# Optimization experiments

Measured on AMD Instinct MI355X. Metric: run time of the kernel, lower is better.

Reference implementation:

```python
import jax, jax.numpy as jnp
import numpy as np

NUM_HEADS = 16
EPS = 1e-6


def _phi(x):
    # Positive feature map: ELU + 1
    return jax.nn.elu(x) + 1.0


def setup_inputs() -> dict:
    key = jax.random.key(0)
    ks = jax.random.split(key, 5)
    B, L, D = 4, 8192, 1024
    scale = 0.02
    return {
        "x": jax.random.normal(ks[0], (B, L, D), dtype=jnp.float32),
        "Wq": jax.random.normal(ks[1], (D, D), dtype=jnp.float32) * scale,
        "Wk": jax.random.normal(ks[2], (D, D), dtype=jnp.float32) * scale,
        "Wv": jax.random.normal(ks[3], (D, D), dtype=jnp.float32) * scale,
        "Wo": jax.random.normal(ks[4], (D, D), dtype=jnp.float32) * scale,
    }


def reference(x, Wq, Wk, Wv, Wo):
    B, L, D = x.shape
    H = NUM_HEADS
    dh = D // H
    # Projections (bias-free linear layers)
    Q = x @ Wq
    K = x @ Wk
    V = x @ Wv
    # Split heads: (B, H, L, dh)
    Qh = Q.reshape(B, L, H, dh).transpose(0, 2, 1, 3)
    Kh = K.reshape(B, L, H, dh).transpose(0, 2, 1, 3)
    Vh = V.reshape(B, L, H, dh).transpose(0, 2, 1, 3)
    Qf = _phi(Qh)
    Kf = _phi(Kh)
    # Global key-value reduction over time: (B, H, dh, dh)
    Kv = jnp.einsum('bhlm,bhln->bhmn', Kf, Vh)
    # Key normalizer: (B, H, dh)
    K1 = jnp.sum(Kf, axis=2)
    # Numerator / denominator
    num = jnp.einsum('bhlm,bhmn->bhln', Qf, Kv)
    den = jnp.einsum('bhlm,bhm->bhl', Qf, K1) + EPS
    out = num / den[..., None]
    out = out.transpose(0, 2, 1, 3).reshape(B, L, D)
    return out @ Wo
```

## Files before the change

### kernel.cpp

```cpp
#include <hip/hip_runtime.h>
#include <stdint.h>
#include <stddef.h>

typedef __bf16 bf16;
typedef __attribute__((ext_vector_type(8))) __bf16 bf16x8;
typedef __attribute__((ext_vector_type(4))) __bf16 bf16x4;
typedef __attribute__((ext_vector_type(4))) float f32x4;

#define ATT_EPS 1e-6f

__device__ __forceinline__ void lds16(const void* g, void* l) {
    __builtin_amdgcn_global_load_lds(
        (const __attribute__((address_space(1))) void*)g,
        (__attribute__((address_space(3))) void*)l, 16, 0, 0);
}

__global__ __launch_bounds__(256) void cvt_bf16(const float4* __restrict__ in,
                                                bf16x4* __restrict__ out, int n4) {
    int i = blockIdx.x * 256 + threadIdx.x;
    if (i < n4) {
        float4 v = in[i];
        bf16x4 o;
        o.x = (bf16)v.x; o.y = (bf16)v.y; o.z = (bf16)v.z; o.w = (bf16)v.w;
        out[i] = o;
    }
}

__global__ __launch_bounds__(256) void transpose_w(const float* __restrict__ W,
                                                   bf16* __restrict__ Wt) {
    __shared__ float tile[32][33];
    const int bx = blockIdx.x * 32, by = blockIdx.y * 32;
    const int tx = threadIdx.x, ty = threadIdx.y;
#pragma unroll
    for (int j = 0; j < 32; j += 8)
        tile[ty + j][tx] = W[(size_t)(by + ty + j) * 1024 + bx + tx];
    __syncthreads();
#pragma unroll
    for (int j = 0; j < 32; j += 8)
        Wt[(size_t)(bx + ty + j) * 1024 + by + tx] = (bf16)tile[tx][ty + j];
}

template <int MODE>
__global__ __launch_bounds__(512) void gemm256(const bf16* __restrict__ A, int lda,
                                               const bf16* __restrict__ B, int ldb,
                                               void* __restrict__ C, int ldc,
                                               int K, int fast_m, int fl2) {
    __shared__ bf16 smem[65536] __attribute__((aligned(16)));
    const int t = threadIdx.x;
    const int wave = t >> 6, lane = t & 63;
    const int q8 = gridDim.x >> 3;
    const int wg = (blockIdx.x & 7) * q8 + (blockIdx.x >> 3);
    const int f = wg & ((1 << fl2) - 1), s = wg >> fl2;
    const int mt = fast_m ? f : s, nt = fast_m ? s : f;
    const int tileM = mt << 8, tileN = nt << 8;
    const int wm = wave >> 2, wn = wave & 3;

    int rowS[2], colS[2];
#pragma unroll
    for (int j = 0; j < 2; j++) {
        int off = t * 16 + j * 8192;
        int o = off & 1023;
        int op = o ^ (((o >> 9) & 1) << 5);
        rowS[j] = (off >> 10) * 16 + (op >> 6);
        colS[j] = (op & 63) >> 1;
    }
    const int rm = lane & 15, qq = lane >> 4;
    const int foff = ((rm * 64 + qq * 16) ^ ((rm >> 3) << 5)) >> 1;

    const bf16* gA0 = A + (size_t)(tileM + rowS[0]) * lda + colS[0];
    const bf16* gA1 = A + (size_t)(tileM + rowS[1]) * lda + colS[1];
    const bf16* gB0 = B + (size_t)(tileN + rowS[0]) * ldb + colS[0];
    const bf16* gB1 = B + (size_t)(tileN + rowS[1]) * ldb + colS[1];

    f32x4 acc[8][4] = {};

#define STAGE(tt)                                                              \
    {                                                                          \
        bf16* base_ = smem + ((tt) & 3) * 16384;                               \
        const int k0_ = (tt) << 5;                                             \
        lds16(gA0 + k0_, base_ + wave * 512);                                  \
        lds16(gA1 + k0_, base_ + 4096 + wave * 512);                           \
        lds16(gB0 + k0_, base_ + 8192 + wave * 512);                           \
        lds16(gB1 + k0_, base_ + 12288 + wave * 512);                          \
    }

#define PHASE(tt, DOSTG, VM)                                                   \
    {                                                                          \
        const bf16* pA_ = smem + ((tt) & 3) * 16384 + wm * 4096 + foff;        \
        const bf16* pB_ = smem + ((tt) & 3) * 16384 + 8192 + wn * 2048 + foff; \
        bf16x8 af_[8], bv_[4];                                                 \
        _Pragma("unroll") for (int mi = 0; mi < 8; mi++)                       \
            af_[mi] = *(const bf16x8*)(pA_ + mi * 512);                        \
        _Pragma("unroll") for (int ni = 0; ni < 4; ni++)                       \
            bv_[ni] = *(const bf16x8*)(pB_ + ni * 512);                        \
        if (DOSTG) STAGE((tt) + 3);                                            \
        asm volatile("s_waitcnt vmcnt(" #VM ")" ::: "memory");                 \
        __builtin_amdgcn_s_barrier();                                          \
        asm volatile("s_waitcnt lgkmcnt(0)" ::: "memory");                     \
        __builtin_amdgcn_s_setprio(1);                                         \
        _Pragma("unroll") for (int mi = 0; mi < 8; mi++)                       \
            _Pragma("unroll") for (int ni = 0; ni < 4; ni++)                   \
                acc[mi][ni] = __builtin_amdgcn_mfma_f32_16x16x32_bf16(         \
                    af_[mi], bv_[ni], acc[mi][ni], 0, 0, 0);                   \
        __builtin_amdgcn_s_setprio(0);                                         \
        __builtin_amdgcn_s_barrier();                                          \
    }

    const int NT = K >> 5;
    STAGE(0); STAGE(1); STAGE(2);
    asm volatile("s_waitcnt vmcnt(8)" ::: "memory");
    __builtin_amdgcn_s_barrier();
    for (int tt = 0; tt < NT - 3; ++tt)
        PHASE(tt, 1, 8);
    PHASE(NT - 3, 0, 4);
    PHASE(NT - 2, 0, 0);
    PHASE(NT - 1, 0, 0);
#undef STAGE
#undef PHASE

    const int row0 = (lane >> 4) * 4, col = lane & 15;
    if (MODE == 0) {
        float* Cf = (float*)C;
#pragma unroll
        for (int mi = 0; mi < 8; mi++)
#pragma unroll
            for (int ni = 0; ni < 4; ni++)
#pragma unroll
                for (int r = 0; r < 4; r++) {
                    int gm = tileM + wm * 128 + mi * 16 + row0 + r;
                    int gn = tileN + wn * 64 + ni * 16 + col;
                    Cf[(size_t)gm * ldc + gn] = acc[mi][ni][r];
                }
    } else {
        bf16* Cb = (bf16*)C;
#pragma unroll
        for (int mi = 0; mi < 8; mi++)
#pragma unroll
            for (int ni = 0; ni < 4; ni++)
#pragma unroll
                for (int r = 0; r < 4; r++) {
                    float v = acc[mi][ni][r];
                    if (MODE == 2) v = (v > 0.f) ? (v + 1.f) : __expf(v);
                    smem[(wm * 128 + mi * 16 + row0 + r) * 256 +
                         wn * 64 + ni * 16 + col] = (bf16)v;
                }
        __syncthreads();
#pragma unroll
        for (int i = 0; i < 16; i++) {
            int c = t + i * 512;
            int row = c >> 5, cb = (c & 31) * 8;
            *(bf16x8*)&Cb[(size_t)(tileM + row) * ldc + tileN + cb] =
                *(const bf16x8*)&smem[row * 256 + cb];
        }
    }
}

__global__ __launch_bounds__(256) void kv_reduce(const bf16* __restrict__ Kft,
                                                 const bf16* __restrict__ Vt,
                                                 float* __restrict__ Kv) {
    const int chunk = blockIdx.x;
    const int bh = blockIdx.y;
    const int b = bh >> 4, h = bh & 15;
    __shared__ bf16 sA[64 * 32] __attribute__((aligned(16)));
    __shared__ bf16 sB[64 * 32] __attribute__((aligned(16)));
    const int t = threadIdx.x, wave = t >> 6, lane = t & 63;
    const size_t cbase = (size_t)b * 8192 + (size_t)chunk * 1024;
    const int srow = t >> 2, scol = (t & 3) * 8;
    const bf16* a0 = Kft + (size_t)(h * 64 + srow) * 32768 + cbase + scol;
    const bf16* b0 = Vt + (size_t)(h * 64 + srow) * 32768 + cbase + scol;
    bf16* dA = sA + wave * 512;
    bf16* dB = sB + wave * 512;
    const int rm = lane & 15, qk = (lane >> 4) * 8;

    f32x4 acc[4] = {};
    f32x4 acc1 = {0.f, 0.f, 0.f, 0.f};
    bf16x8 ones;
#pragma unroll
    for (int j = 0; j < 8; j++) ones[j] = (bf16)1.0f;

    for (int k0 = 0; k0 < 1024; k0 += 32) {
        lds16(a0 + k0, dA);
        lds16(b0 + k0, dB);
        __builtin_amdgcn_s_waitcnt(0);
        __syncthreads();
        bf16x8 af = *(const bf16x8*)&sA[(wave * 16 + rm) * 32 + qk];
        bf16x8 bfr[4];
#pragma unroll
        for (int ni = 0; ni < 4; ni++)
            bfr[ni] = *(const bf16x8*)&sB[(ni * 16 + rm) * 32 + qk];
#pragma unroll
        for (int ni = 0; ni < 4; ni++)
            acc[ni] = __builtin_amdgcn_mfma_f32_16x16x32_bf16(af, bfr[ni], acc[ni], 0, 0, 0);
        acc1 = __builtin_amdgcn_mfma_f32_16x16x32_bf16(af, ones, acc1, 0, 0, 0);
        __syncthreads();
    }

    float* out = Kv + bh * 65 * 64;
    const int row0 = (lane >> 4) * 4, col = lane & 15;
    const int m0 = wave * 16 + row0;
#pragma unroll
    for (int ni = 0; ni < 4; ni++)
#pragma unroll
        for (int r = 0; r < 4; r++)
            atomicAdd(&out[(ni * 16 + col) * 64 + m0 + r], acc[ni][r]);
    if (col == 0) {
#pragma unroll
        for (int r = 0; r < 4; r++) atomicAdd(&out[64 * 64 + m0 + r], acc1[r]);
    }
}

__global__ __launch_bounds__(256) void attn_out(const bf16* __restrict__ Qf,
                                                const float* __restrict__ Kv,
                                                bf16* __restrict__ attn) {
    const int lt = blockIdx.x;
    const int bh = blockIdx.y;
    const int b = bh >> 4, h = bh & 15;
    constexpr int EP_STRIDE = 80;
    __shared__ bf16 smem[13312] __attribute__((aligned(16)));
    __shared__ float den[128];
    bf16* sQ = smem;
    bf16* sB = smem + 8192;
    const int t = threadIdx.x, wave = t >> 6, lane = t & 63;
    const int qrow = t >> 3, qc = (t & 7) * 8;
    const bf16* qp = Qf + (size_t)(b * 8192 + lt * 128 + qrow) * 1024 + h * 64 + qc;
#pragma unroll
    for (int i = 0; i < 4; i++)
        lds16(qp + (size_t)i * 32 * 1024, sQ + i * 2048 + wave * 512);
    const float* kv = Kv + bh * 65 * 64;
    for (int idx = t; idx < 80 * 64; idx += 256) {
        int n = idx >> 6, k2 = idx & 63;
        sB[idx] = (n < 65) ? (bf16)kv[n * 64 + k2] : (bf16)0.f;
    }
    __builtin_amdgcn_s_waitcnt(0);
    __syncthreads();

    f32x4 acc[2][5] = {};
    const int rm = lane & 15, qk = (lane >> 4) * 8;
#pragma unroll
    for (int k0 = 0; k0 < 64; k0 += 32) {
        bf16x8 af[2], bfr[5];
#pragma unroll
        for (int mi = 0; mi < 2; mi++)
            af[mi] = *(const bf16x8*)&sQ[(wave * 32 + mi * 16 + rm) * 64 + k0 + qk];
#pragma unroll
        for (int ni = 0; ni < 5; ni++)
            bfr[ni] = *(const bf16x8*)&sB[(ni * 16 + rm) * 64 + k0 + qk];
#pragma unroll
        for (int mi = 0; mi < 2; mi++)
#pragma unroll
            for (int ni = 0; ni < 5; ni++)
                acc[mi][ni] = __builtin_amdgcn_mfma_f32_16x16x32_bf16(
                    af[mi], bfr[ni], acc[mi][ni], 0, 0, 0);
    }

    const int row0 = (lane >> 4) * 4, col = lane & 15;
    if (col == 0) {
#pragma unroll
        for (int mi = 0; mi < 2; mi++)
#pragma unroll
            for (int r = 0; r < 4; r++)
                den[wave * 32 + mi * 16 + row0 + r] = acc[mi][4][r] + ATT_EPS;
    }
    __syncthreads();
#pragma unroll
    for (int mi = 0; mi < 2; mi++)
#pragma unroll
        for (int ni = 0; ni < 4; ni++)
#pragma unroll
            for (int r = 0; r < 4; r++) {
                int rl = wave * 32 + mi * 16 + row0 + r;
                smem[rl * EP_STRIDE + ni * 16 + col] =
                    (bf16)(acc[mi][ni][r] / den[rl]);
            }
    __syncthreads();
    const int er = t >> 3, ec = (t & 7) * 8;
#pragma unroll
    for (int i = 0; i < 4; i++) {
        int row = er + i * 32;
        *(bf16x8*)&attn[(size_t)(b * 8192 + lt * 128 + row) * 1024 + h * 64 + ec] =
            *(const bf16x8*)&smem[row * EP_STRIDE + ec];
    }
}

extern "C" void kernel_launch(void* const* d_in, const int* in_sizes, int n_in,
                              void* d_out, int out_size, void* d_ws, size_t ws_size,
                              hipStream_t stream) {
    const float* x  = (const float*)d_in[0];
    const float* Wq = (const float*)d_in[1];
    const float* Wk = (const float*)d_in[2];
    const float* Wv = (const float*)d_in[3];
    const float* Wo = (const float*)d_in[4];

    char* ws = (char*)d_ws;
    bf16* xb  = (bf16*)ws;
    bf16* Qf  = (bf16*)(ws + ((size_t)64 << 20));
    bf16* Kft = (bf16*)(ws + ((size_t)128 << 20));
    bf16* Vt  = (bf16*)(ws + ((size_t)192 << 20));
    bf16* Wqt = (bf16*)(ws + ((size_t)256 << 20));
    bf16* Wkt = Wqt + 1024 * 1024;
    bf16* Wvt = Wkt + 1024 * 1024;
    bf16* Wot = Wvt + 1024 * 1024;
    float* Kv = (float*)(Wot + 1024 * 1024);
    bf16* attn = xb;

    cvt_bf16<<<8388608 / 256, 256, 0, stream>>>((const float4*)x, (bf16x4*)xb, 8388608);
    dim3 tb(32, 8);
    transpose_w<<<dim3(32, 32), tb, 0, stream>>>(Wq, Wqt);
    transpose_w<<<dim3(32, 32), tb, 0, stream>>>(Wk, Wkt);
    transpose_w<<<dim3(32, 32), tb, 0, stream>>>(Wv, Wvt);
    transpose_w<<<dim3(32, 32), tb, 0, stream>>>(Wo, Wot);
    hipMemsetAsync(Kv, 0, (size_t)64 * 65 * 64 * sizeof(float), stream);

    gemm256<2><<<512, 512, 0, stream>>>(xb, 1024, Wqt, 1024, Qf, 1024, 1024, 0, 2);
    gemm256<2><<<512, 512, 0, stream>>>(Wkt, 1024, xb, 1024, Kft, 32768, 1024, 1, 2);
    gemm256<1><<<512, 512, 0, stream>>>(Wvt, 1024, xb, 1024, Vt, 32768, 1024, 1, 2);
    kv_reduce<<<dim3(8, 64), 256, 0, stream>>>(Kft, Vt, Kv);
    attn_out<<<dim3(64, 64), 256, 0, stream>>>(Qf, Kv, attn);
    gemm256<0><<<512, 512, 0, stream>>>(attn, 1024, Wot, 1024, d_out, 1024, 1024, 0, 2);
}
```

Baseline: 653.5 us.

## Shrink GEMM tile to 256x128 and double-buffer LDS fragment reads in registers

The GEMM tile changes from 256x256 to 256x128, which doubles the grid to 1024 workgroups and cuts LDS use from 128KB to 96KB. Each wave now owns a 64x64 output region. The LDS-to-register fragment loads for the next k-step are issued right after the barrier and overlap the current step's MFMAs, using two register sets that alternate. The main loop drops to one barrier per phase. The trade-off is less data reuse per tile and more global traffic, in exchange for better occupancy and load/compute overlap.

```diff
diff --git a/kernel.cpp b/kernel.cpp
--- a/kernel.cpp
+++ b/kernel.cpp
@@ -41,80 +41,97 @@
 }
 
 template <int MODE>
-__global__ __launch_bounds__(512) void gemm256(const bf16* __restrict__ A, int lda,
+__global__ __launch_bounds__(512) void gemm_px(const bf16* __restrict__ A, int lda,
                                                const bf16* __restrict__ B, int ldb,
                                                void* __restrict__ C, int ldc,
                                                int K, int fast_m, int fl2) {
-    __shared__ bf16 smem[65536] __attribute__((aligned(16)));
+    __shared__ bf16 smem[49152] __attribute__((aligned(16)));
     const int t = threadIdx.x;
     const int wave = t >> 6, lane = t & 63;
     const int q8 = gridDim.x >> 3;
     const int wg = (blockIdx.x & 7) * q8 + (blockIdx.x >> 3);
     const int f = wg & ((1 << fl2) - 1), s = wg >> fl2;
     const int mt = fast_m ? f : s, nt = fast_m ? s : f;
-    const int tileM = mt << 8, tileN = nt << 8;
-    const int wm = wave >> 2, wn = wave & 3;
-
-    int rowS[2], colS[2];
+    const int tileM = mt << 8, tileN = nt << 7;
+    const int wm = wave >> 1, wn = wave & 1;
+
+    int rA[2], cA[2], rB, cB;
 #pragma unroll
     for (int j = 0; j < 2; j++) {
-        int off = t * 16 + j * 8192;
-        int o = off & 1023;
-        int op = o ^ (((o >> 9) & 1) << 5);
-        rowS[j] = (off >> 10) * 16 + (op >> 6);
-        colS[j] = (op & 63) >> 1;
-    }
+        int ol = t * 16 + j * 8192;
+        int o = ol & 1023, op = o ^ (((o >> 9) & 1) << 5);
+        rA[j] = ((ol >> 10) << 4) | (op >> 6);
+        cA[j] = (op & 63) >> 1;
+    }
+    {
+        int ol = t * 16;
+        int o = ol & 1023, op = o ^ (((o >> 9) & 1) << 5);
+        rB = ((ol >> 10) << 4) | (op >> 6);
+        cB = (op & 63) >> 1;
+    }
+    const bf16* gA0 = A + (size_t)(tileM + rA[0]) * lda + cA[0];
+    const bf16* gA1 = A + (size_t)(tileM + rA[1]) * lda + cA[1];
+    const bf16* gB0 = B + (size_t)(tileN + rB) * ldb + cB;
+
     const int rm = lane & 15, qq = lane >> 4;
-    const int foff = ((rm * 64 + qq * 16) ^ ((rm >> 3) << 5)) >> 1;
-
-    const bf16* gA0 = A + (size_t)(tileM + rowS[0]) * lda + colS[0];
-    const bf16* gA1 = A + (size_t)(tileM + rowS[1]) * lda + colS[1];
-    const bf16* gB0 = B + (size_t)(tileN + rowS[0]) * ldb + colS[0];
-    const bf16* gB1 = B + (size_t)(tileN + rowS[1]) * ldb + colS[1];
-
-    f32x4 acc[8][4] = {};
+    const int foffE = ((rm * 64 + qq * 16) ^ ((rm >> 3) << 5)) >> 1;
+
+    f32x4 acc[4][4] = {};
+    bf16x8 af0[4], bv0[4], af1[4], bv1[4];
 
 #define STAGE(tt)                                                              \
     {                                                                          \
-        bf16* base_ = smem + ((tt) & 3) * 16384;                               \
-        const int k0_ = (tt) << 5;                                             \
-        lds16(gA0 + k0_, base_ + wave * 512);                                  \
-        lds16(gA1 + k0_, base_ + 4096 + wave * 512);                           \
-        lds16(gB0 + k0_, base_ + 8192 + wave * 512);                           \
-        lds16(gB1 + k0_, base_ + 12288 + wave * 512);                          \
-    }
-
-#define PHASE(tt, DOSTG, VM)                                                   \
+        bf16* b_ = smem + ((tt) & 3) * 12288;                                  \
+        const int k_ = (tt) << 5;                                              \
+        lds16(gA0 + k_, b_ + wave * 512);                                      \
+        lds16(gA1 + k_, b_ + 4096 + wave * 512);                               \
+        lds16(gB0 + k_, b_ + 8192 + wave * 512);                               \
+    }
+
+#define PHASE(tt, afR, bvR, afW, bvW, DOSTG, VM, DORD)                         \
     {                                                                          \
-        const bf16* pA_ = smem + ((tt) & 3) * 16384 + wm * 4096 + foff;        \
-        const bf16* pB_ = smem + ((tt) & 3) * 16384 + 8192 + wn * 2048 + foff; \
-        bf16x8 af_[8], bv_[4];                                                 \
-        _Pragma("unroll") for (int mi = 0; mi < 8; mi++)                       \
-            af_[mi] = *(const bf16x8*)(pA_ + mi * 512);                        \
-        _Pragma("unroll") for (int ni = 0; ni < 4; ni++)                       \
-            bv_[ni] = *(const bf16x8*)(pB_ + ni * 512);                        \
         if (DOSTG) STAGE((tt) + 3);                                            \
         asm volatile("s_waitcnt vmcnt(" #VM ")" ::: "memory");                 \
-        __builtin_amdgcn_s_barrier();                                          \
         asm volatile("s_waitcnt lgkmcnt(0)" ::: "memory");                     \
+        asm volatile("s_barrier" ::: "memory");                                \
+        if (DORD) {                                                            \
+            const bf16* pA_ =                                                  \
+                smem + (((tt) + 1) & 3) * 12288 + wm * 2048 + foffE;           \
+            const bf16* pB_ =                                                  \
+                smem + (((tt) + 1) & 3) * 12288 + 8192 + wn * 2048 + foffE;    \
+            _Pragma("unroll") for (int mi = 0; mi < 4; mi++)                   \
+                afW[mi] = *(const bf16x8*)(pA_ + mi * 512);                    \
+            _Pragma("unroll") for (int ni = 0; ni < 4; ni++)                   \
+                bvW[ni] = *(const bf16x8*)(pB_ + ni * 512);                    \
+        }                                                                      \
         __builtin_amdgcn_s_setprio(1);                                         \
-        _Pragma("unroll") for (int mi = 0; mi < 8; mi++)                       \
+        _Pragma("unroll") for (int mi = 0; mi < 4; mi++)                       \
             _Pragma("unroll") for (int ni = 0; ni < 4; ni++)                   \
                 acc[mi][ni] = __builtin_amdgcn_mfma_f32_16x16x32_bf16(         \
-                    af_[mi], bv_[ni], acc[mi][ni], 0, 0, 0);                   \
+                    afR[mi], bvR[ni], acc[mi][ni], 0, 0, 0);                   \
         __builtin_amdgcn_s_setprio(0);                                         \
-        __builtin_amdgcn_s_barrier();                                          \
     }
 
     const int NT = K >> 5;
     STAGE(0); STAGE(1); STAGE(2);
-    asm volatile("s_waitcnt vmcnt(8)" ::: "memory");
-    __builtin_amdgcn_s_barrier();
-    for (int tt = 0; tt < NT - 3; ++tt)
-        PHASE(tt, 1, 8);
-    PHASE(NT - 3, 0, 4);
-    PHASE(NT - 2, 0, 0);
-    PHASE(NT - 1, 0, 0);
+    asm volatile("s_waitcnt vmcnt(6)" ::: "memory");
+    asm volatile("s_barrier" ::: "memory");
+    {
+        const bf16* pA_ = smem + wm * 2048 + foffE;
+        const bf16* pB_ = smem + 8192 + wn * 2048 + foffE;
+#pragma unroll
+        for (int mi = 0; mi < 4; mi++) af0[mi] = *(const bf16x8*)(pA_ + mi * 512);
+#pragma unroll
+        for (int ni = 0; ni < 4; ni++) bv0[ni] = *(const bf16x8*)(pB_ + ni * 512);
+    }
+    for (int tt = 0; tt < NT - 4; tt += 2) {
+        PHASE(tt,     af0, bv0, af1, bv1, 1, 6, 1);
+        PHASE(tt + 1, af1, bv1, af0, bv0, 1, 6, 1);
+    }
+    PHASE(NT - 4, af0, bv0, af1, bv1, 1, 6, 1);
+    PHASE(NT - 3, af1, bv1, af0, bv0, 0, 3, 1);
+    PHASE(NT - 2, af0, bv0, af1, bv1, 0, 0, 1);
+    PHASE(NT - 1, af1, bv1, af0, bv0, 0, 0, 0);
 #undef STAGE
 #undef PHASE
 
@@ -122,35 +139,35 @@
     if (MODE == 0) {
         float* Cf = (float*)C;
 #pragma unroll
-        for (int mi = 0; mi < 8; mi++)
+        for (int mi = 0; mi < 4; mi++)
 #pragma unroll
             for (int ni = 0; ni < 4; ni++)
 #pragma unroll
                 for (int r = 0; r < 4; r++) {
-                    int gm = tileM + wm * 128 + mi * 16 + row0 + r;
+                    int gm = tileM + wm * 64 + mi * 16 + row0 + r;
                     int gn = tileN + wn * 64 + ni * 16 + col;
                     Cf[(size_t)gm * ldc + gn] = acc[mi][ni][r];
                 }
     } else {
         bf16* Cb = (bf16*)C;
 #pragma unroll
-        for (int mi = 0; mi < 8; mi++)
+        for (int mi = 0; mi < 4; mi++)
 #pragma unroll
             for (int ni = 0; ni < 4; ni++)
 #pragma unroll
                 for (int r = 0; r < 4; r++) {
                     float v = acc[mi][ni][r];
                     if (MODE == 2) v = (v > 0.f) ? (v + 1.f) : __expf(v);
-                    smem[(wm * 128 + mi * 16 + row0 + r) * 256 +
+                    smem[(wm * 64 + mi * 16 + row0 + r) * 128 +
                          wn * 64 + ni * 16 + col] = (bf16)v;
                 }
         __syncthreads();
 #pragma unroll
-        for (int i = 0; i < 16; i++) {
+        for (int i = 0; i < 8; i++) {
             int c = t + i * 512;
-            int row = c >> 5, cb = (c & 31) * 8;
+            int row = c >> 4, cb = (c & 15) * 8;
             *(bf16x8*)&Cb[(size_t)(tileM + row) * ldc + tileN + cb] =
-                *(const bf16x8*)&smem[row * 256 + cb];
+                *(const bf16x8*)&smem[row * 128 + cb];
         }
     }
 }
@@ -311,10 +328,10 @@
     transpose_w<<<dim3(32, 32), tb, 0, stream>>>(Wo, Wot);
     hipMemsetAsync(Kv, 0, (size_t)64 * 65 * 64 * sizeof(float), stream);
 
-    gemm256<2><<<512, 512, 0, stream>>>(xb, 1024, Wqt, 1024, Qf, 1024, 1024, 0, 2);
-    gemm256<2><<<512, 512, 0, stream>>>(Wkt, 1024, xb, 1024, Kft, 32768, 1024, 1, 2);
-    gemm256<1><<<512, 512, 0, stream>>>(Wvt, 1024, xb, 1024, Vt, 32768, 1024, 1, 2);
+    gemm_px<2><<<1024, 512, 0, stream>>>(xb, 1024, Wqt, 1024, Qf, 1024, 1024, 0, 3);
+    gemm_px<2><<<1024, 512, 0, stream>>>(Wkt, 1024, xb, 1024, Kft, 32768, 1024, 1, 2);
+    gemm_px<1><<<1024, 512, 0, stream>>>(Wvt, 1024, xb, 1024, Vt, 32768, 1024, 1, 2);
     kv_reduce<<<dim3(8, 64), 256, 0, stream>>>(Kft, Vt, Kv);
     attn_out<<<dim3(64, 64), 256, 0, stream>>>(Qf, Kv, attn);
-    gemm256<0><<<512, 512, 0, stream>>>(attn, 1024, Wot, 1024, d_out, 1024, 1024, 0, 2);
-}
+    gemm_px<0><<<1024, 512, 0, stream>>>(attn, 1024, Wot, 1024, d_out, 1024, 1024, 0, 3);
+}
```

Result: slower. 702.0 us (+7.4%).

## Restructure GEMM mainloop into 8-phase double-buffered schedule with K=64 tiles

Applied to the files above, without the earlier changes.

Replaces the 4-stage, K=32 LDS ring in the 256x256 GEMM with a double-buffered K=64 tile, split into four sub-phases per tile. Each sub-phase loads half of the A fragments and issues one quarter of the next tile's global->LDS copies, so loads and MFMA work are interleaved at finer granularity. It also changes the LDS swizzle to a row-major 32-element layout with an XOR on the column chunk. This aims to cut register pressure and hide load latency better. The cost is twice as many barriers per K step, plus a new swizzle that could bring back bank conflicts.

```diff
diff --git a/kernel.cpp b/kernel.cpp
--- a/kernel.cpp
+++ b/kernel.cpp
@@ -41,10 +41,10 @@
 }
 
 template <int MODE>
-__global__ __launch_bounds__(512) void gemm256(const bf16* __restrict__ A, int lda,
-                                               const bf16* __restrict__ B, int ldb,
-                                               void* __restrict__ C, int ldc,
-                                               int K, int fast_m, int fl2) {
+__global__ __launch_bounds__(512) void gemm8p(const bf16* __restrict__ A, int lda,
+                                              const bf16* __restrict__ B, int ldb,
+                                              void* __restrict__ C, int ldc,
+                                              int K, int fast_m, int fl2) {
     __shared__ bf16 smem[65536] __attribute__((aligned(16)));
     const int t = threadIdx.x;
     const int wave = t >> 6, lane = t & 63;
@@ -55,67 +55,68 @@
     const int tileM = mt << 8, tileN = nt << 8;
     const int wm = wave >> 2, wn = wave & 3;
 
-    int rowS[2], colS[2];
-#pragma unroll
-    for (int j = 0; j < 2; j++) {
-        int off = t * 16 + j * 8192;
-        int o = off & 1023;
-        int op = o ^ (((o >> 9) & 1) << 5);
-        rowS[j] = (off >> 10) * 16 + (op >> 6);
-        colS[j] = (op & 63) >> 1;
-    }
+    const int sRow = t >> 2;
+    const int sc = (((t & 3) * 16) ^ (((sRow >> 1) & 3) << 4)) >> 1;
+    const bf16* gA0 = A + (size_t)(tileM + sRow) * lda + sc;
+    const bf16* gA1 = A + (size_t)(tileM + 128 + sRow) * lda + sc;
+    const bf16* gB0 = B + (size_t)(tileN + sRow) * ldb + sc;
+    const bf16* gB1 = B + (size_t)(tileN + 128 + sRow) * ldb + sc;
+
     const int rm = lane & 15, qq = lane >> 4;
-    const int foff = ((rm * 64 + qq * 16) ^ ((rm >> 3) << 5)) >> 1;
-
-    const bf16* gA0 = A + (size_t)(tileM + rowS[0]) * lda + colS[0];
-    const bf16* gA1 = A + (size_t)(tileM + rowS[1]) * lda + colS[1];
-    const bf16* gB0 = B + (size_t)(tileN + rowS[0]) * ldb + colS[0];
-    const bf16* gB1 = B + (size_t)(tileN + rowS[1]) * ldb + colS[1];
+    const int cx = (qq ^ ((rm >> 1) & 3)) * 8;
 
     f32x4 acc[8][4] = {};
-
-#define STAGE(tt)                                                              \
+    bf16x8 af[4], bv[4];
+
+#define STG(tt, it)                                                            \
     {                                                                          \
-        bf16* base_ = smem + ((tt) & 3) * 16384;                               \
-        const int k0_ = (tt) << 5;                                             \
-        lds16(gA0 + k0_, base_ + wave * 512);                                  \
-        lds16(gA1 + k0_, base_ + 4096 + wave * 512);                           \
-        lds16(gB0 + k0_, base_ + 8192 + wave * 512);                           \
-        lds16(gB1 + k0_, base_ + 12288 + wave * 512);                          \
-    }
-
-#define PHASE(tt, DOSTG, VM)                                                   \
+        bf16* d_ = smem + ((tt) & 1) * 32768 + (it) * 8192 + wave * 512;       \
+        const int ko_ = (tt) * 64 + ((it) >> 1) * 32;                          \
+        lds16((((it) & 1) ? gB0 : gA0) + ko_, d_);                             \
+        lds16((((it) & 1) ? gB1 : gA1) + ko_, d_ + 4096);                      \
+    }
+
+#define PHASE(tt, p, DOSTG, VM)                                                \
     {                                                                          \
-        const bf16* pA_ = smem + ((tt) & 3) * 16384 + wm * 4096 + foff;        \
-        const bf16* pB_ = smem + ((tt) & 3) * 16384 + 8192 + wn * 2048 + foff; \
-        bf16x8 af_[8], bv_[4];                                                 \
-        _Pragma("unroll") for (int mi = 0; mi < 8; mi++)                       \
-            af_[mi] = *(const bf16x8*)(pA_ + mi * 512);                        \
-        _Pragma("unroll") for (int ni = 0; ni < 4; ni++)                       \
-            bv_[ni] = *(const bf16x8*)(pB_ + ni * 512);                        \
-        if (DOSTG) STAGE((tt) + 3);                                            \
+        constexpr int kk_ = (p) >> 1, mh_ = (p) & 1;                           \
+        const bf16* as_ = smem + ((tt) & 1) * 32768 + kk_ * 16384;             \
+        const bf16* bs_ = as_ + 8192;                                          \
+        if (mh_ == 0) {                                                        \
+            _Pragma("unroll") for (int ni = 0; ni < 4; ni++)                   \
+                bv[ni] = *(const bf16x8*)(bs_ + (wn * 64 + ni * 16 + rm) * 32  \
+                                          + cx);                               \
+        }                                                                      \
+        _Pragma("unroll") for (int mi = 0; mi < 4; mi++)                       \
+            af[mi] = *(const bf16x8*)(as_ +                                    \
+                (wm * 128 + (mh_ * 4 + mi) * 16 + rm) * 32 + cx);              \
+        if (DOSTG) STG((tt) + 1, p);                                           \
         asm volatile("s_waitcnt vmcnt(" #VM ")" ::: "memory");                 \
-        __builtin_amdgcn_s_barrier();                                          \
+        asm volatile("s_barrier" ::: "memory");                                \
         asm volatile("s_waitcnt lgkmcnt(0)" ::: "memory");                     \
         __builtin_amdgcn_s_setprio(1);                                         \
-        _Pragma("unroll") for (int mi = 0; mi < 8; mi++)                       \
+        _Pragma("unroll") for (int mi = 0; mi < 4; mi++)                       \
             _Pragma("unroll") for (int ni = 0; ni < 4; ni++)                   \
-                acc[mi][ni] = __builtin_amdgcn_mfma_f32_16x16x32_bf16(         \
-                    af_[mi], bv_[ni], acc[mi][ni], 0, 0, 0);                   \
+                acc[mh_ * 4 + mi][ni] = __builtin_amdgcn_mfma_f32_16x16x32_bf16(\
+                    af[mi], bv[ni], acc[mh_ * 4 + mi][ni], 0, 0, 0);           \
         __builtin_amdgcn_s_setprio(0);                                         \
-        __builtin_amdgcn_s_barrier();                                          \
-    }
-
-    const int NT = K >> 5;
-    STAGE(0); STAGE(1); STAGE(2);
-    asm volatile("s_waitcnt vmcnt(8)" ::: "memory");
-    __builtin_amdgcn_s_barrier();
-    for (int tt = 0; tt < NT - 3; ++tt)
-        PHASE(tt, 1, 8);
-    PHASE(NT - 3, 0, 4);
-    PHASE(NT - 2, 0, 0);
-    PHASE(NT - 1, 0, 0);
-#undef STAGE
+        asm volatile("s_barrier" ::: "memory");                                \
+    }
+
+    const int NKT = K >> 6;
+    STG(0, 0); STG(0, 1); STG(0, 2); STG(0, 3);
+    asm volatile("s_waitcnt vmcnt(4)" ::: "memory");
+    asm volatile("s_barrier" ::: "memory");
+    for (int tt = 0; tt < NKT - 1; ++tt) {
+        PHASE(tt, 0, 1, 4);
+        PHASE(tt, 1, 1, 4);
+        PHASE(tt, 2, 1, 4);
+        PHASE(tt, 3, 1, 4);
+    }
+    PHASE(NKT - 1, 0, 0, 2);
+    PHASE(NKT - 1, 1, 0, 0);
+    PHASE(NKT - 1, 2, 0, 0);
+    PHASE(NKT - 1, 3, 0, 0);
+#undef STG
 #undef PHASE
 
     const int row0 = (lane >> 4) * 4, col = lane & 15;
@@ -311,10 +312,10 @@
     transpose_w<<<dim3(32, 32), tb, 0, stream>>>(Wo, Wot);
     hipMemsetAsync(Kv, 0, (size_t)64 * 65 * 64 * sizeof(float), stream);
 
-    gemm256<2><<<512, 512, 0, stream>>>(xb, 1024, Wqt, 1024, Qf, 1024, 1024, 0, 2);
-    gemm256<2><<<512, 512, 0, stream>>>(Wkt, 1024, xb, 1024, Kft, 32768, 1024, 1, 2);
-    gemm256<1><<<512, 512, 0, stream>>>(Wvt, 1024, xb, 1024, Vt, 32768, 1024, 1, 2);
+    gemm8p<2><<<512, 512, 0, stream>>>(xb, 1024, Wqt, 1024, Qf, 1024, 1024, 0, 2);
+    gemm8p<2><<<512, 512, 0, stream>>>(Wkt, 1024, xb, 1024, Kft, 32768, 1024, 1, 2);
+    gemm8p<1><<<512, 512, 0, stream>>>(Wvt, 1024, xb, 1024, Vt, 32768, 1024, 1, 2);
     kv_reduce<<<dim3(8, 64), 256, 0, stream>>>(Kft, Vt, Kv);
     attn_out<<<dim3(64, 64), 256, 0, stream>>>(Qf, Kv, attn);
-    gemm256<0><<<512, 512, 0, stream>>>(attn, 1024, Wot, 1024, d_out, 1024, 1024, 0, 2);
-}
+    gemm8p<0><<<512, 512, 0, stream>>>(attn, 1024, Wot, 1024, d_out, 1024, 1024, 0, 2);
+}
```

Result: no change. 646.6 us (-1.0%).
